# Optimization experiments

Measured on AMD Instinct MI355X. Metric: run time of the kernel, lower is better.

## Reference

```python
import jax, jax.numpy as jnp
import numpy as np

N = 100000      # nodes
E = 1_600_000   # edges (avg degree 16)
IN = 128
HID = 128
OUT = 64
C = 7           # num classes == K clusters
BETA = 1.0
NEG_SLOPE = 0.2


def setup_inputs() -> dict:
    key = jax.random.key(0)
    ks = jax.random.split(key, 12)
    x = jax.random.normal(ks[0], (N, IN), jnp.float32)
    edge_index = jax.random.randint(ks[1], (2, E), 0, N, dtype=jnp.int32)
    y = jax.random.randint(ks[2], (N,), 0, C, dtype=jnp.int32)
    C_b_prime = jax.random.normal(ks[3], (C, IN), jnp.float32)
    Q = jax.random.uniform(ks[4], (C, C), jnp.float32, 0.1, 1.0)  # positive, log-safe
    s1 = 1.0 / np.sqrt(IN)
    s2 = 1.0 / np.sqrt(HID)
    W1 = jax.random.uniform(ks[5], (IN, HID), jnp.float32, -s1, s1)
    a_src1 = jax.random.uniform(ks[6], (HID,), jnp.float32, -s2, s2)
    a_dst1 = jax.random.uniform(ks[7], (HID,), jnp.float32, -s2, s2)
    b1 = jnp.zeros((HID,), jnp.float32)
    W2 = jax.random.uniform(ks[8], (HID, OUT), jnp.float32, -s2, s2)
    b2 = jnp.zeros((OUT,), jnp.float32)
    return dict(x=x, edge_index=edge_index, y=y, C_b_prime=C_b_prime, Q=Q,
                W1=W1, a_src1=a_src1, a_dst1=a_dst1, b1=b1, W2=W2, b2=b2)


def _segment_softmax(logits, seg, num):
    m = jax.ops.segment_max(logits, seg, num_segments=num)
    e = jnp.exp(logits - m[seg])
    s = jax.ops.segment_sum(e, seg, num_segments=num)
    return e / (s[seg] + 1e-16)


def _clust_score(feat, cent, beta=BETA):
    # get_clust_score_pytorch: softmax-normalized exp(-beta * ||f - c_k||)
    d = jnp.linalg.norm(feat[:, None, :] - cent[None, :, :], axis=2)  # [N,K]
    sc = jnp.exp(-beta * d) + 1e-10
    return sc / sc.sum(1, keepdims=True)


def _gat_layer1(x, W, a_src, a_dst, b, src, dst):
    h = x @ W                                                   # F_0: [N,HID]
    logits = jax.nn.leaky_relu(h[src] @ a_src + h[dst] @ a_dst, NEG_SLOPE)  # [E]
    alpha = _segment_softmax(logits, dst, N)                    # B_0: [E]
    out = jax.ops.segment_sum(alpha[:, None] * h[src], dst, num_segments=N) + b  # Z_0
    return out, alpha, h


def reference(x, edge_index, y, C_b_prime, Q, W1, a_src1, a_dst1, b1, W2, b2):
    src, dst = edge_index[0], edge_index[1]

    # conv1 (GAT, heads=1) with return_attention_weights
    Z0, B0, F0 = _gat_layer1(x, W1, a_src1, a_dst1, b1, src, dst)
    x1 = jax.nn.elu(Z0)  # dropout p=0.5 in eval mode -> identity

    # ---- get_grad_IB_B_large ----
    y1h = jax.nn.one_hot(y, C, dtype=x.dtype)
    # run_kmeans(Z, y, C) replaced by detached class-mean centroids
    cnt = jax.ops.segment_sum(jnp.ones((N,), x.dtype), y, num_segments=C)
    C_a = jax.lax.stop_gradient(
        jax.ops.segment_sum(Z0, y, num_segments=C) / (cnt[:, None] + 1e-12))
    phi_Z = jax.lax.stop_gradient(_clust_score(Z0, C_a))      # [N,C], detached
    phi_X = _clust_score(x, C_b_prime)                        # [N,C]
    S = jnp.log(phi_X).sum(1)                                 # sum_b log phi_X_b
    diff_b = phi_Z * S[:, None] - y1h @ jnp.log(Q)            # [N,C]
    # U = d phi_Z / d Z (softmax-of-neg-distance Jacobian)
    dZ = Z0[:, None, :] - C_a[None, :, :]                     # [N,C,HID]
    dist = jnp.linalg.norm(dZ, axis=2, keepdims=True) + 1e-12
    g = -BETA * dZ / dist
    U = phi_Z[..., None] * (g - jnp.sum(phi_Z[..., None] * g, axis=1, keepdims=True))
    v = jnp.einsum('nkd,nk->nd', U, diff_b)                   # [N,HID]
    # grad_IB_B0[src,dst] = (v @ F0.T)[src,dst]/N, gathered per edge (no NxN dense)
    grad_e = jnp.einsum('ed,ed->e', v[src], F0[dst]) / N      # [E]

    B1 = B0 - grad_e
    # torch: B_1.norm(p=2, dim=1, keepdim=True) on [E,1] == |B_1| per edge, detached
    B1 = B1 / jax.lax.stop_gradient(jnp.abs(B1) + 1e-16)

    # conv2 with provided attention_weights B1
    h2 = x1 @ W2                                              # Z_1: [N,OUT]
    out = jax.ops.segment_sum(B1[:, None] * h2[src], dst, num_segments=N) + b2
    return out, h2, Z0, phi_Z
```

## Files before the change

kernel.cpp:

```cpp
#include <hip/hip_runtime.h>
#include <hip/hip_bf16.h>
#include <math.h>

#define IN_DIM 128
#define HID_DIM 128
#define OUT_DIM 64
#define NCLS 7

__global__ __launch_bounds__(256) void gemm1_kernel(
    const float* __restrict__ x, const float* __restrict__ W1,
    float* __restrict__ F0, int n) {
  __shared__ float xs[64 * 128];
  const int t = threadIdx.x;
  const int n0 = blockIdx.x * 64;

  for (int i = t; i < 64 * 128; i += 256) {
    int r = i >> 7, cc = i & 127;
    int gr = n0 + r;
    xs[i] = (gr < n) ? x[(size_t)gr * 128 + cc] : 0.0f;
  }
  __syncthreads();

  const int c = t & 127;
  const int half = t >> 7;
  float acc[32];
#pragma unroll
  for (int i = 0; i < 32; i++) acc[i] = 0.0f;

  for (int k0 = 0; k0 < 128; k0 += 8) {
    float w[8];
#pragma unroll
    for (int kk = 0; kk < 8; kk++) w[kk] = W1[(size_t)(k0 + kk) * 128 + c];
#pragma unroll
    for (int i = 0; i < 32; i++) {
      const int r = half + 2 * i;
#pragma unroll
      for (int kk = 0; kk < 8; kk++) acc[i] += xs[r * 128 + k0 + kk] * w[kk];
    }
  }
#pragma unroll
  for (int i = 0; i < 32; i++) {
    int gr = n0 + half + 2 * i;
    if (gr < n) F0[(size_t)gr * 128 + c] = acc[i];
  }
}

__global__ __launch_bounds__(256) void dots_kernel(
    const float* __restrict__ F0, const float* __restrict__ a_src,
    const float* __restrict__ a_dst, float* __restrict__ as_dot,
    float* __restrict__ ad_dot, int n) {
  const int wid = (blockIdx.x * blockDim.x + threadIdx.x) >> 6;
  const int lane = threadIdx.x & 63;
  if (wid >= n) return;
  float f0 = F0[(size_t)wid * 128 + lane];
  float f1 = F0[(size_t)wid * 128 + 64 + lane];
  float s = f0 * a_src[lane] + f1 * a_src[64 + lane];
  float d = f0 * a_dst[lane] + f1 * a_dst[64 + lane];
  for (int m = 32; m; m >>= 1) {
    s += __shfl_xor(s, m);
    d += __shfl_xor(d, m);
  }
  if (lane == 0) {
    as_dot[wid] = s;
    ad_dot[wid] = d;
  }
}

__global__ __launch_bounds__(256) void hist_kernel(const int* __restrict__ dst,
                                                   int* __restrict__ deg,
                                                   int e) {
  int i = blockIdx.x * blockDim.x + threadIdx.x;
  if (i < e) atomicAdd(&deg[dst[i]], 1);
}

__global__ __launch_bounds__(256) void scan1_kernel(const int* __restrict__ deg,
                                                    int* __restrict__ bsum,
                                                    int n) {
  __shared__ int lds[256];
  const int b = blockIdx.x, t = threadIdx.x;
  const int base = b * 1024 + t * 4;
  int s = 0;
#pragma unroll
  for (int u = 0; u < 4; u++) {
    int i = base + u;
    if (i < n) s += deg[i];
  }
  lds[t] = s;
  __syncthreads();
  for (int off = 128; off; off >>= 1) {
    if (t < off) lds[t] += lds[t + off];
    __syncthreads();
  }
  if (t == 0) bsum[b] = lds[0];
}

__global__ __launch_bounds__(1024) void scan2_kernel(
    const int* __restrict__ bsum, int* __restrict__ boff,
    int* __restrict__ rowptr, int nb, int n) {
  __shared__ int lds[1024];
  const int t = threadIdx.x;
  int v = (t < nb) ? bsum[t] : 0;
  lds[t] = v;
  __syncthreads();
  for (int off = 1; off < 1024; off <<= 1) {
    int add = (t >= off) ? lds[t - off] : 0;
    __syncthreads();
    lds[t] += add;
    __syncthreads();
  }
  if (t < nb) boff[t] = lds[t] - v;
  if (t == nb - 1) rowptr[n] = lds[t];
}

__global__ __launch_bounds__(256) void scan3_kernel(
    const int* __restrict__ deg, const int* __restrict__ boff,
    int* __restrict__ rowptr, int* __restrict__ cursor, int n) {
  __shared__ int lds[256];
  const int b = blockIdx.x, t = threadIdx.x;
  const int base = b * 1024 + t * 4;
  int v[4];
  int s = 0;
#pragma unroll
  for (int u = 0; u < 4; u++) {
    int i = base + u;
    v[u] = (i < n) ? deg[i] : 0;
    s += v[u];
  }
  lds[t] = s;
  __syncthreads();
  for (int off = 1; off < 256; off <<= 1) {
    int add = (t >= off) ? lds[t - off] : 0;
    __syncthreads();
    lds[t] += add;
    __syncthreads();
  }
  int run = boff[b] + lds[t] - s;
#pragma unroll
  for (int u = 0; u < 4; u++) {
    int i = base + u;
    if (i < n) {
      rowptr[i] = run;
      cursor[i] = run;
      run += v[u];
    }
  }
}

__global__ __launch_bounds__(256) void scatter_kernel(
    const int* __restrict__ src, const int* __restrict__ dst,
    int* __restrict__ cursor, int* __restrict__ esrc, int e) {
  int i = blockIdx.x * blockDim.x + threadIdx.x;
  if (i < e) {
    int pos = atomicAdd(&cursor[dst[i]], 1);
    esrc[pos] = src[i];
  }
}

__global__ __launch_bounds__(256) void gat1_kernel(
    const float* __restrict__ F0, const float* __restrict__ as_dot,
    const float* __restrict__ ad_dot, const int* __restrict__ rowptr,
    const int* __restrict__ esrc, const float* __restrict__ b1,
    float* __restrict__ alpha, float* __restrict__ Z0out, int n) {
  const int wid = (blockIdx.x * blockDim.x + threadIdx.x) >> 6;
  const int lane = threadIdx.x & 63;
  if (wid >= n) return;
  const int start = rowptr[wid];
  const int end = rowptr[wid + 1];
  const float adn = ad_dot[wid];

  float lmax = -INFINITY;
  for (int j = start + lane; j < end; j += 64) {
    int s = esrc[j];
    float z = as_dot[s] + adn;
    z = (z > 0.0f) ? z : 0.2f * z;
    lmax = fmaxf(lmax, z);
  }
  for (int m = 32; m; m >>= 1) lmax = fmaxf(lmax, __shfl_xor(lmax, m));

  float lsum = 0.0f;
  for (int j = start + lane; j < end; j += 64) {
    int s = esrc[j];
    float z = as_dot[s] + adn;
    z = (z > 0.0f) ? z : 0.2f * z;
    lsum += expf(z - lmax);
  }
  for (int m = 32; m; m >>= 1) lsum += __shfl_xor(lsum, m);
  const float inv = 1.0f / (lsum + 1e-16f);

  const int g = lane >> 4;
  const int l = lane & 15;
  float4 accA = {0.f, 0.f, 0.f, 0.f};
  float4 accB = {0.f, 0.f, 0.f, 0.f};
  for (int base = start; base < end; base += 4) {
    const int j = base + g;
    const bool act = (j < end);
    const int sj = act ? esrc[j] : 0;
    float aj = 0.0f;
    if (act) {
      float z = as_dot[sj] + adn;
      z = (z > 0.0f) ? z : 0.2f * z;
      aj = expf(z - lmax) * inv;
      if (l == 0) alpha[j] = aj;
    }
    const float4 vA = *(const float4*)&F0[(size_t)sj * 128 + l * 8];
    const float4 vB = *(const float4*)&F0[(size_t)sj * 128 + l * 8 + 4];
    accA.x += aj * vA.x; accA.y += aj * vA.y;
    accA.z += aj * vA.z; accA.w += aj * vA.w;
    accB.x += aj * vB.x; accB.y += aj * vB.y;
    accB.z += aj * vB.z; accB.w += aj * vB.w;
  }
#pragma unroll
  for (int m = 16; m <= 32; m <<= 1) {
    accA.x += __shfl_xor(accA.x, m); accA.y += __shfl_xor(accA.y, m);
    accA.z += __shfl_xor(accA.z, m); accA.w += __shfl_xor(accA.w, m);
    accB.x += __shfl_xor(accB.x, m); accB.y += __shfl_xor(accB.y, m);
    accB.z += __shfl_xor(accB.z, m); accB.w += __shfl_xor(accB.w, m);
  }
  if (g == 0) {
    const float4 bA = *(const float4*)&b1[l * 8];
    const float4 bB = *(const float4*)&b1[l * 8 + 4];
    float4 oA = {accA.x + bA.x, accA.y + bA.y, accA.z + bA.z, accA.w + bA.w};
    float4 oB = {accB.x + bB.x, accB.y + bB.y, accB.z + bB.z, accB.w + bB.w};
    *(float4*)&Z0out[(size_t)wid * 128 + l * 8] = oA;
    *(float4*)&Z0out[(size_t)wid * 128 + l * 8 + 4] = oB;
  }
}

#define CNB 256
__global__ __launch_bounds__(128) void centroid_partial_kernel(
    const float* __restrict__ Z0out, const int* __restrict__ y,
    float* __restrict__ partial, float* __restrict__ ccnt, int n, int per) {
  const int t = threadIdx.x;
  const int b = blockIdx.x;
  const int n0 = b * per;
  const int n1 = min(n0 + per, n);
  float a[NCLS];
#pragma unroll
  for (int k = 0; k < NCLS; k++) a[k] = 0.0f;
  int cnt[NCLS];
#pragma unroll
  for (int k = 0; k < NCLS; k++) cnt[k] = 0;

#pragma unroll 4
  for (int i = n0; i < n1; i++) {
    const int c = y[i];
    const float v = Z0out[(size_t)i * 128 + t];
#pragma unroll
    for (int k = 0; k < NCLS; k++) a[k] += (c == k) ? v : 0.0f;
    if (t == 0) {
#pragma unroll
      for (int k = 0; k < NCLS; k++) cnt[k] += (c == k) ? 1 : 0;
    }
  }
#pragma unroll
  for (int k = 0; k < NCLS; k++)
    partial[((size_t)b * NCLS + k) * 128 + t] = a[k];
  if (t == 0) {
#pragma unroll
    for (int k = 0; k < NCLS; k++) atomicAdd(&ccnt[k], (float)cnt[k]);
  }
}

__global__ __launch_bounds__(1024) void centroid_reduce_kernel(
    const float* __restrict__ partial, const float* __restrict__ ccnt,
    float* __restrict__ ca, int nb) {
  const int t = threadIdx.x;
  if (t >= NCLS * 128) return;
  float s = 0.0f;
#pragma unroll 8
  for (int b = 0; b < nb; b++) s += partial[(size_t)b * (NCLS * 128) + t];
  ca[t] = s / (ccnt[t >> 7] + 1e-12f);
}

__global__ __launch_bounds__(256) void phi_v_kernel(
    const float* __restrict__ Z0out, const float* __restrict__ x,
    const float* __restrict__ ca, const float* __restrict__ cb,
    const float* __restrict__ Q, const int* __restrict__ y,
    float* __restrict__ vbuf, float* __restrict__ phi_out, int n) {
  const int wid = (blockIdx.x * blockDim.x + threadIdx.x) >> 6;
  const int lane = threadIdx.x & 63;
  if (wid >= n) return;
  const float z0 = Z0out[(size_t)wid * 128 + lane];
  const float z1 = Z0out[(size_t)wid * 128 + 64 + lane];
  const float x0 = x[(size_t)wid * 128 + lane];
  const float x1 = x[(size_t)wid * 128 + 64 + lane];

  float sZ[NCLS], sX[NCLS];
#pragma unroll
  for (int k = 0; k < NCLS; k++) {
    float d0 = z0 - ca[k * 128 + lane];
    float d1 = z1 - ca[k * 128 + 64 + lane];
    sZ[k] = d0 * d0 + d1 * d1;
    float e0 = x0 - cb[k * 128 + lane];
    float e1 = x1 - cb[k * 128 + 64 + lane];
    sX[k] = e0 * e0 + e1 * e1;
  }
  for (int m = 32; m; m >>= 1) {
#pragma unroll
    for (int k = 0; k < NCLS; k++) {
      sZ[k] += __shfl_xor(sZ[k], m);
      sX[k] += __shfl_xor(sX[k], m);
    }
  }
  float distZ[NCLS], phiZ[NCLS];
  float sumZ = 0.0f, sumX = 0.0f, S = 0.0f;
#pragma unroll
  for (int k = 0; k < NCLS; k++) {
    distZ[k] = sqrtf(sZ[k]);
    float sc = expf(-distZ[k]) + 1e-10f;
    phiZ[k] = sc;
    sumZ += sc;
    float dx = sqrtf(sX[k]);
    float scx = expf(-dx) + 1e-10f;
    S += logf(scx);
    sumX += scx;
  }
  S -= 7.0f * logf(sumX);
  const float invZ = 1.0f / sumZ;
#pragma unroll
  for (int k = 0; k < NCLS; k++) phiZ[k] *= invZ;

  const int yc = y[wid];
  float w[NCLS];
  float W = 0.0f;
#pragma unroll
  for (int k = 0; k < NCLS; k++) {
    float diff = phiZ[k] * S - logf(Q[yc * NCLS + k]);
    w[k] = phiZ[k] * diff;
    W += w[k];
  }
  float v0 = 0.0f, v1 = 0.0f;
#pragma unroll
  for (int k = 0; k < NCLS; k++) {
    float coef = -(w[k] - W * phiZ[k]) / (distZ[k] + 1e-12f);
    v0 += coef * (z0 - ca[k * 128 + lane]);
    v1 += coef * (z1 - ca[k * 128 + 64 + lane]);
  }
  vbuf[(size_t)wid * 128 + lane] = v0;
  vbuf[(size_t)wid * 128 + 64 + lane] = v1;

  if (lane < NCLS) {
    float pv = (lane == 0) ? phiZ[0]
              : (lane == 1) ? phiZ[1]
              : (lane == 2) ? phiZ[2]
              : (lane == 3) ? phiZ[3]
              : (lane == 4) ? phiZ[4]
              : (lane == 5) ? phiZ[5]
                            : phiZ[6];
    phi_out[(size_t)wid * NCLS + lane] = pv;
  }
}

__global__ __launch_bounds__(256) void gemm2_kernel(
    const float* __restrict__ Z0out, const float* __restrict__ W2,
    float* __restrict__ h2, int n) {
  __shared__ float w2s[128 * 64];
  __shared__ float xs[16 * 128];
  const int t = threadIdx.x;
  for (int i = t; i < 128 * 64; i += 256) w2s[i] = W2[i];
  const int n0 = blockIdx.x * 16;
  for (int i = t; i < 16 * 128; i += 256) {
    int r = i >> 7, cc = i & 127;
    int gr = n0 + r;
    float zv = (gr < n) ? Z0out[(size_t)gr * 128 + cc] : 0.0f;
    xs[i] = (zv > 0.0f) ? zv : (expf(zv) - 1.0f);
  }
  __syncthreads();
  const int c = t & 63;
  const int rb = t >> 6;
  float acc[4] = {0.0f, 0.0f, 0.0f, 0.0f};
  for (int k = 0; k < 128; k++) {
    float wv = w2s[k * 64 + c];
#pragma unroll
    for (int i = 0; i < 4; i++) acc[i] += xs[(rb + 4 * i) * 128 + k] * wv;
  }
#pragma unroll
  for (int i = 0; i < 4; i++) {
    int gr = n0 + rb + 4 * i;
    if (gr < n) h2[(size_t)gr * 64 + c] = acc[i];
  }
}

__global__ __launch_bounds__(256) void conv2_kernel(
    const float* __restrict__ F0, const float* __restrict__ vbuf,
    const float* __restrict__ h2, const float* __restrict__ alpha,
    const int* __restrict__ rowptr, const int* __restrict__ esrc,
    const float* __restrict__ b2, float* __restrict__ outp, int n,
    float invN) {
  const int wid = (blockIdx.x * blockDim.x + threadIdx.x) >> 6;
  const int lane = threadIdx.x & 63;
  if (wid >= n) return;
  const int start = rowptr[wid];
  const int end = rowptr[wid + 1];
  const int g = lane >> 4;
  const int l = lane & 15;
  const float4 fA = *(const float4*)&F0[(size_t)wid * 128 + l * 8];
  const float4 fB = *(const float4*)&F0[(size_t)wid * 128 + l * 8 + 4];
  float acc = 0.0f;
  for (int base = start; base < end; base += 4) {
    const int j = base + g;
    const bool act = (j < end);
    const int sj = act ? esrc[j] : 0;
    const float a = act ? alpha[j] : 0.0f;
    const float4 vA = *(const float4*)&vbuf[(size_t)sj * 128 + l * 8];
    const float4 vB = *(const float4*)&vbuf[(size_t)sj * 128 + l * 8 + 4];
    float p = vA.x * fA.x + vA.y * fA.y + vA.z * fA.z + vA.w * fA.w +
              vB.x * fB.x + vB.y * fB.y + vB.z * fB.z + vB.w * fB.w;
    p += __shfl_xor(p, 1);
    p += __shfl_xor(p, 2);
    p += __shfl_xor(p, 4);
    p += __shfl_xor(p, 8);
    const float B1 = a - p * invN;
    const float w = act ? (B1 / (fabsf(B1) + 1e-16f)) : 0.0f;
#pragma unroll
    for (int g2 = 0; g2 < 4; g2++) {
      const float wg = __shfl(w, g2 * 16);
      const int sg = __shfl(sj, g2 * 16);
      acc += wg * h2[(size_t)sg * 64 + lane];
    }
  }
  outp[(size_t)wid * 64 + lane] = acc + b2[lane];
}

extern "C" void kernel_launch(void* const* d_in, const int* in_sizes, int n_in,
                              void* d_out, int out_size, void* d_ws,
                              size_t ws_size, hipStream_t stream) {
  const float* x = (const float*)d_in[0];
  const int* ei = (const int*)d_in[1];
  const int* y = (const int*)d_in[2];
  const float* cb = (const float*)d_in[3];
  const float* Q = (const float*)d_in[4];
  const float* W1 = (const float*)d_in[5];
  const float* a_src = (const float*)d_in[6];
  const float* a_dst = (const float*)d_in[7];
  const float* b1 = (const float*)d_in[8];
  const float* W2 = (const float*)d_in[9];
  const float* b2 = (const float*)d_in[10];

  const int N = in_sizes[2];
  const int E = in_sizes[1] / 2;
  const int* srcp = ei;
  const int* dstp = ei + E;

  float* F0 = (float*)d_ws;
  float* as_dot = F0 + (size_t)N * 128;
  float* ad_dot = as_dot + N;
  float* alpha = ad_dot + N;
  float* vbuf = alpha + E;
  float* ca = vbuf + (size_t)N * 128;
  float* ccnt = ca + NCLS * 128;
  int* deg = (int*)(ccnt + 16);
  int* rowptr = deg + N;
  int* cursor = rowptr + N + 1;
  int* esrc = cursor + N;

  float* partial = vbuf;
  int* bsum = (int*)(vbuf + (size_t)CNB * NCLS * 128);
  int* boff = bsum + 1024;

  float* out_o = (float*)d_out;
  float* h2_o = out_o + (size_t)N * 64;
  float* z0_o = h2_o + (size_t)N * 64;
  float* phi_o = z0_o + (size_t)N * 128;

  hipMemsetAsync(deg, 0, (size_t)N * sizeof(int), stream);
  hipMemsetAsync(ccnt, 0, 16 * sizeof(float), stream);

  gemm1_kernel<<<(N + 63) / 64, 256, 0, stream>>>(x, W1, F0, N);
  dots_kernel<<<(N + 3) / 4, 256, 0, stream>>>(F0, a_src, a_dst, as_dot,
                                               ad_dot, N);
  hist_kernel<<<(E + 255) / 256, 256, 0, stream>>>(dstp, deg, E);
  {
    const int nb = (N + 1023) / 1024;
    scan1_kernel<<<nb, 256, 0, stream>>>(deg, bsum, N);
    scan2_kernel<<<1, 1024, 0, stream>>>(bsum, boff, rowptr, nb, N);
    scan3_kernel<<<nb, 256, 0, stream>>>(deg, boff, rowptr, cursor, N);
  }
  scatter_kernel<<<(E + 255) / 256, 256, 0, stream>>>(srcp, dstp, cursor, esrc,
                                                      E);
  gat1_kernel<<<(N + 3) / 4, 256, 0, stream>>>(F0, as_dot, ad_dot, rowptr,
                                               esrc, b1, alpha, z0_o, N);
  {
    const int per = (N + CNB - 1) / CNB;
    centroid_partial_kernel<<<CNB, 128, 0, stream>>>(z0_o, y, partial, ccnt, N,
                                                     per);
    centroid_reduce_kernel<<<1, 1024, 0, stream>>>(partial, ccnt, ca, CNB);
  }
  phi_v_kernel<<<(N + 3) / 4, 256, 0, stream>>>(z0_o, x, ca, cb, Q, y, vbuf,
                                                phi_o, N);
  gemm2_kernel<<<(N + 15) / 16, 256, 0, stream>>>(z0_o, W2, h2_o, N);
  conv2_kernel<<<(N + 3) / 4, 256, 0, stream>>>(F0, vbuf, h2_o, alpha, rowptr,
                                                esrc, b2, out_o, N,
                                                1.0f / (float)N);
}
```

Before: 1.030 ms.

## Add single-pass low-degree GAT path, widen conv2 edge batching, split centroid reduce

The GAT layer-1 kernel gets a fast path for nodes with degree at most 64. Each lane holds one edge, the softmax is done with wave shuffles in a single pass, and the neighbour rows are aggregated eight edges at a time with float4 loads, so esrc and as_dot are no longer re-read across several passes. conv2 now handles eight edges per iteration with eight lanes per edge dot product, and it skips h2 loads when the edge weight is zero. The centroid reduction is spread over seven blocks, one per class, instead of one 1024-thread block. Register pressure in both kernels rises from the wider float4 accumulators.

New measurement: 1.059 ms. +2.8%, slower.

```diff
diff --git a/kernel.cpp b/kernel.cpp
--- a/kernel.cpp
+++ b/kernel.cpp
@@ -166,7 +166,75 @@
   if (wid >= n) return;
   const int start = rowptr[wid];
   const int end = rowptr[wid + 1];
+  const int deg = end - start;
   const float adn = ad_dot[wid];
+
+  if (deg <= 64) {
+    const int j = start + lane;
+    const bool act = (j < end);
+    const int sj = act ? esrc[j] : 0;
+    float z = -INFINITY;
+    if (act) {
+      z = as_dot[sj] + adn;
+      z = (z > 0.0f) ? z : 0.2f * z;
+    }
+    float lmax = z;
+    for (int m = 32; m; m >>= 1) lmax = fmaxf(lmax, __shfl_xor(lmax, m));
+    const float ez = act ? expf(z - lmax) : 0.0f;
+    float lsum = ez;
+    for (int m = 32; m; m >>= 1) lsum += __shfl_xor(lsum, m);
+    const float aj = ez * (1.0f / (lsum + 1e-16f));
+    if (act) alpha[j] = aj;
+
+    const int g = lane >> 3;
+    const int l = lane & 7;
+    float4 a0 = {0.f, 0.f, 0.f, 0.f}, a1 = {0.f, 0.f, 0.f, 0.f};
+    float4 a2v = {0.f, 0.f, 0.f, 0.f}, a3 = {0.f, 0.f, 0.f, 0.f};
+    for (int base = 0; base < deg; base += 8) {
+      const int e = base + g;
+      const float we = __shfl(aj, e);
+      const int se = __shfl(sj, e);
+      if (e < deg) {
+        const float* fr = &F0[(size_t)se * 128 + l * 16];
+        const float4 u0 = *(const float4*)(fr);
+        const float4 u1 = *(const float4*)(fr + 4);
+        const float4 u2 = *(const float4*)(fr + 8);
+        const float4 u3 = *(const float4*)(fr + 12);
+        a0.x += we * u0.x; a0.y += we * u0.y; a0.z += we * u0.z; a0.w += we * u0.w;
+        a1.x += we * u1.x; a1.y += we * u1.y; a1.z += we * u1.z; a1.w += we * u1.w;
+        a2v.x += we * u2.x; a2v.y += we * u2.y; a2v.z += we * u2.z; a2v.w += we * u2.w;
+        a3.x += we * u3.x; a3.y += we * u3.y; a3.z += we * u3.z; a3.w += we * u3.w;
+      }
+    }
+#pragma unroll
+    for (int m = 8; m <= 32; m <<= 1) {
+      a0.x += __shfl_xor(a0.x, m); a0.y += __shfl_xor(a0.y, m);
+      a0.z += __shfl_xor(a0.z, m); a0.w += __shfl_xor(a0.w, m);
+      a1.x += __shfl_xor(a1.x, m); a1.y += __shfl_xor(a1.y, m);
+      a1.z += __shfl_xor(a1.z, m); a1.w += __shfl_xor(a1.w, m);
+      a2v.x += __shfl_xor(a2v.x, m); a2v.y += __shfl_xor(a2v.y, m);
+      a2v.z += __shfl_xor(a2v.z, m); a2v.w += __shfl_xor(a2v.w, m);
+      a3.x += __shfl_xor(a3.x, m); a3.y += __shfl_xor(a3.y, m);
+      a3.z += __shfl_xor(a3.z, m); a3.w += __shfl_xor(a3.w, m);
+    }
+    if (g == 0) {
+      const float* bp = &b1[l * 16];
+      const float4 c0 = *(const float4*)(bp);
+      const float4 c1 = *(const float4*)(bp + 4);
+      const float4 c2 = *(const float4*)(bp + 8);
+      const float4 c3 = *(const float4*)(bp + 12);
+      float* op = &Z0out[(size_t)wid * 128 + l * 16];
+      float4 o0 = {a0.x + c0.x, a0.y + c0.y, a0.z + c0.z, a0.w + c0.w};
+      float4 o1 = {a1.x + c1.x, a1.y + c1.y, a1.z + c1.z, a1.w + c1.w};
+      float4 o2 = {a2v.x + c2.x, a2v.y + c2.y, a2v.z + c2.z, a2v.w + c2.w};
+      float4 o3 = {a3.x + c3.x, a3.y + c3.y, a3.z + c3.z, a3.w + c3.w};
+      *(float4*)(op) = o0;
+      *(float4*)(op + 4) = o1;
+      *(float4*)(op + 8) = o2;
+      *(float4*)(op + 12) = o3;
+    }
+    return;
+  }
 
   float lmax = -INFINITY;
   for (int j = start + lane; j < end; j += 64) {
@@ -261,15 +329,16 @@
   }
 }
 
-__global__ __launch_bounds__(1024) void centroid_reduce_kernel(
+__global__ __launch_bounds__(128) void centroid_reduce_kernel(
     const float* __restrict__ partial, const float* __restrict__ ccnt,
     float* __restrict__ ca, int nb) {
+  const int k = blockIdx.x;
   const int t = threadIdx.x;
-  if (t >= NCLS * 128) return;
   float s = 0.0f;
 #pragma unroll 8
-  for (int b = 0; b < nb; b++) s += partial[(size_t)b * (NCLS * 128) + t];
-  ca[t] = s / (ccnt[t >> 7] + 1e-12f);
+  for (int b = 0; b < nb; b++)
+    s += partial[((size_t)b * NCLS + k) * 128 + t];
+  ca[k * 128 + t] = s / (ccnt[k] + 1e-12f);
 }
 
 __global__ __launch_bounds__(256) void phi_v_kernel(
@@ -392,31 +461,41 @@
   if (wid >= n) return;
   const int start = rowptr[wid];
   const int end = rowptr[wid + 1];
-  const int g = lane >> 4;
-  const int l = lane & 15;
-  const float4 fA = *(const float4*)&F0[(size_t)wid * 128 + l * 8];
-  const float4 fB = *(const float4*)&F0[(size_t)wid * 128 + l * 8 + 4];
+  const int g = lane >> 3;
+  const int l = lane & 7;
+  float4 f0_[4];
+#pragma unroll
+  for (int u = 0; u < 4; u++)
+    f0_[u] = *(const float4*)&F0[(size_t)wid * 128 + l * 16 + u * 4];
   float acc = 0.0f;
-  for (int base = start; base < end; base += 4) {
+  for (int base = start; base < end; base += 8) {
     const int j = base + g;
     const bool act = (j < end);
     const int sj = act ? esrc[j] : 0;
     const float a = act ? alpha[j] : 0.0f;
-    const float4 vA = *(const float4*)&vbuf[(size_t)sj * 128 + l * 8];
-    const float4 vB = *(const float4*)&vbuf[(size_t)sj * 128 + l * 8 + 4];
-    float p = vA.x * fA.x + vA.y * fA.y + vA.z * fA.z + vA.w * fA.w +
-              vB.x * fB.x + vB.y * fB.y + vB.z * fB.z + vB.w * fB.w;
+    const float* vr = &vbuf[(size_t)sj * 128 + l * 16];
+    const float4 v0 = *(const float4*)(vr);
+    const float4 v1 = *(const float4*)(vr + 4);
+    const float4 v2 = *(const float4*)(vr + 8);
+    const float4 v3 = *(const float4*)(vr + 12);
+    float p = v0.x * f0_[0].x + v0.y * f0_[0].y + v0.z * f0_[0].z +
+              v0.w * f0_[0].w + v1.x * f0_[1].x + v1.y * f0_[1].y +
+              v1.z * f0_[1].z + v1.w * f0_[1].w + v2.x * f0_[2].x +
+              v2.y * f0_[2].y + v2.z * f0_[2].z + v2.w * f0_[2].w +
+              v3.x * f0_[3].x + v3.y * f0_[3].y + v3.z * f0_[3].z +
+              v3.w * f0_[3].w;
     p += __shfl_xor(p, 1);
     p += __shfl_xor(p, 2);
     p += __shfl_xor(p, 4);
-    p += __shfl_xor(p, 8);
     const float B1 = a - p * invN;
     const float w = act ? (B1 / (fabsf(B1) + 1e-16f)) : 0.0f;
 #pragma unroll
-    for (int g2 = 0; g2 < 4; g2++) {
-      const float wg = __shfl(w, g2 * 16);
-      const int sg = __shfl(sj, g2 * 16);
-      acc += wg * h2[(size_t)sg * 64 + lane];
+    for (int g2 = 0; g2 < 8; g2++) {
+      const float wg = __shfl(w, g2 * 8);
+      if (wg != 0.0f) {
+        const int sg = __shfl(sj, g2 * 8);
+        acc += wg * h2[(size_t)sg * 64 + lane];
+      }
     }
   }
   outp[(size_t)wid * 64 + lane] = acc + b2[lane];
@@ -484,7 +563,7 @@
     const int per = (N + CNB - 1) / CNB;
     centroid_partial_kernel<<<CNB, 128, 0, stream>>>(z0_o, y, partial, ccnt, N,
                                                      per);
-    centroid_reduce_kernel<<<1, 1024, 0, stream>>>(partial, ccnt, ca, CNB);
+    centroid_reduce_kernel<<<NCLS, 128, 0, stream>>>(partial, ccnt, ca, CNB);
   }
   phi_v_kernel<<<(N + 3) / 4, 256, 0, stream>>>(z0_o, x, ca, cb, Q, y, vbuf,
                                                 phi_o, N);
```
